# Optimization experiments

Hardware: AMD Instinct MI355X
Metric: run time of the kernel (lower is better)

Reference implementation:

```python
import jax, jax.numpy as jnp
import numpy as np
from jax import lax

T = 8  # primary_vec_length


def setup_inputs() -> dict:
    key = jax.random.key(0)
    k1, k2, k3 = jax.random.split(key, 3)
    x = jax.random.normal(k1, (32, 256, 64, 64), dtype=jnp.float32)
    # Conv2d weight [out_ch, in_ch, kH, kW], kaiming-ish scale
    W = jax.random.normal(k2, (32, 256, 9, 9), dtype=jnp.float32) * 0.01
    b = jax.random.normal(k3, (32,), dtype=jnp.float32) * 0.01
    return {"x": x, "W": W, "b": b}


def reference(x, W, b):
    B = x.shape[0]
    # Conv2d(kernel=9, stride=2, valid). The original applies this conv T times
    # to identical stacked copies of x; compute it once and broadcast (same math).
    conv = lax.conv_general_dilated(
        x, W, window_strides=(2, 2), padding="VALID",
        dimension_numbers=("NCHW", "OIHW", "NCHW"))
    conv = conv + b[None, :, None, None]            # [B, C, H', W']
    s = jnp.broadcast_to(conv[:, None], (B, T) + conv.shape[1:])  # [B, T, C, H', W']
    # squash along dim=1 (the capsule-vector / time dim)
    sq = jnp.sum(s * s, axis=1, keepdims=True)      # [B, 1, C, H', W']
    scale = sq / (1.0 + sq) / jnp.sqrt(sq + 1e-8)
    squ = s * scale                                  # [B, T, C, H', W']
    squ = squ.reshape(B, T, -1)                      # [B, T, C*H'*W']
    squ = jnp.transpose(squ, (0, 2, 1))[..., None]   # [B, N, T, 1]
    return squ
```

## Files before the change

### kernel.cpp

```cpp
#include <hip/hip_runtime.h>
#include <hip/hip_bf16.h>
#include <stdint.h>

typedef _Float16 f16;
typedef _Float16 f16x8 __attribute__((ext_vector_type(8)));
typedef float f32x16 __attribute__((ext_vector_type(16)));
typedef float f32x4 __attribute__((ext_vector_type(4)));
typedef uint32_t u32x4 __attribute__((ext_vector_type(4)));
typedef uint32_t u32x2 __attribute__((ext_vector_type(2)));

#define MFMA(A, B, C) __builtin_amdgcn_mfma_f32_32x32x16_f16((A), (B), (C), 0, 0, 0)

__global__ __launch_bounds__(256) void nchw_to_nhwc_f16(
    const float* __restrict__ x, f16* __restrict__ xt) {
  __shared__ __align__(16) uint32_t tile[64 * 128];
  const int bh = blockIdx.x;
  const int t = threadIdx.x;
  const float* src = x + (size_t)(bh >> 6) * (256 * 4096) + (bh & 63) * 64;

  const int w4 = t & 15;
  const int cq = t >> 4;
  const int xorv = 4 * (w4 & 7);
#pragma unroll
  for (int it = 0; it < 4; ++it) {
    const int c0 = it * 64 + cq * 4;
    float4 v0 = *(const float4*)(src + (size_t)(c0 + 0) * 4096 + w4 * 4);
    float4 v1 = *(const float4*)(src + (size_t)(c0 + 1) * 4096 + w4 * 4);
    float4 v2 = *(const float4*)(src + (size_t)(c0 + 2) * 4096 + w4 * 4);
    float4 v3 = *(const float4*)(src + (size_t)(c0 + 3) * 4096 + w4 * 4);
    const float* p0 = (const float*)&v0;
    const float* p1 = (const float*)&v1;
    const float* p2 = (const float*)&v2;
    const float* p3 = (const float*)&v3;
    const int u = it * 32 + cq * 2;
#pragma unroll
    for (int jw = 0; jw < 4; ++jw) {
      f16 h0 = (f16)p0[jw], h1 = (f16)p1[jw], h2 = (f16)p2[jw], h3 = (f16)p3[jw];
      uint32_t lo = (uint32_t)__builtin_bit_cast(uint16_t, h0) |
                    ((uint32_t)__builtin_bit_cast(uint16_t, h1) << 16);
      uint32_t hi = (uint32_t)__builtin_bit_cast(uint16_t, h2) |
                    ((uint32_t)__builtin_bit_cast(uint16_t, h3) << 16);
      u32x2 pk = {lo, hi};
      const int w = w4 * 4 + jw;
      *(u32x2*)&tile[w * 128 + (u ^ xorv)] = pk;
    }
  }
  __syncthreads();
  f16* dstb = xt + (size_t)bh * 16384;
#pragma unroll
  for (int it = 0; it < 8; ++it) {
    const int n = it * 256 + t;
    const int w2 = n & 31;
    const int par = (n >> 5) & 1;
    const int g8 = n >> 6;
    const int w = par + 2 * w2;
    const u32x4 v = *(const u32x4*)&tile[w * 128 + ((g8 * 4) ^ (4 * ((w >> 2) & 7)))];
    *(u32x4*)(dstb + n * 8) = v;
  }
}

__global__ __launch_bounds__(256) void pack_w(const float* __restrict__ W,
                                              f16* __restrict__ wt) {
  __shared__ float lds[10368];
  const int t = threadIdx.x;
  const int co = blockIdx.x >> 1;
  const int cih = blockIdx.x & 1;
  const float* src = W + (size_t)(co * 256 + cih * 128) * 81;
  for (int i = t; i < 10368; i += 256) lds[i] = src[i];
  __syncthreads();
  for (int j = t; j < 1296; j += 256) {
    const int kk = j >> 4;
    const int t16 = j & 15;
    const int cicl = t16 >> 2;
    const int sg = t16 & 3;
    const int cin = ((sg >> 1) & 1) * 16 + (sg & 1) * 8;
    f16 tmp[8];
#pragma unroll
    for (int e = 0; e < 8; ++e)
      tmp[e] = (f16)lds[(cicl * 32 + cin + e) * 81 + kk];
    const int cic = cih * 4 + cicl;
    *(f16x8*)&wt[(size_t)(((kk * 8 + cic) * 4 + sg) * 32 + co) * 8] = *(f16x8*)tmp;
  }
}

__global__ __launch_bounds__(256, 2) void conv_direct(
    const f16* __restrict__ xt, const f16* __restrict__ wt,
    float* __restrict__ convp) {
  __shared__ __align__(16) char stg[4 * 18432];
  const int tid = threadIdx.x;
  const int lane = tid & 63;
  const int wave = tid >> 6;
  const int m = lane & 31;
  const int hh = lane >> 5;

  const int blk = blockIdx.x;
  const int xcd = blk & 7;
  const int r = blk >> 3;
  const int i4 = r >> 5;
  const int rr = r & 31;
  const int og = rr >> 3;
  const int cic = rr & 7;
  const int bimg = xcd * 4 + i4;
  const int ohp = og * 4 + wave;
  const bool active = (ohp < 14);

  const char* xb = (const char*)xt;
  const char* wb = (const char*)wt;

  const char* ab = xb + ((size_t)(bimg * 64 + 4 * ohp) * 32768 +
                         cic * 4096 + hh * 1024 + m * 16);
  const size_t cic2048 = (size_t)cic * 2048;
  const int fragoff = hh * 512 + m * 16;

#define GLDS(G, L)                                                            \
  __builtin_amdgcn_global_load_lds(                                           \
      (const __attribute__((address_space(1))) void*)(G),                     \
      (__attribute__((address_space(3))) void*)(L), 16, 0, 0)

#define ALOAD(AB, KW, P) \
  (*(const f16x8*)((AB) + (P) * 2048 + ((KW) & 1) * 512 + ((KW) >> 1) * 16))
#define LDSF(P) (*(const f16x8*)(P))

#define STAGE(JN)                                                             \
  {                                                                           \
    const int kkb = (JN) * 9;                                                 \
    char* db = stg + ((JN) & 3) * 18432;                                      \
    _Pragma("unroll") for (int i = 0; i < 4; ++i) {                           \
      const int u = tid + 256 * i;                                            \
      GLDS(wb + (size_t)(kkb + (u >> 7)) * 16384 + cic2048 + (u & 127) * 16,  \
           db + u * 16);                                                      \
    }                                                                         \
    if (tid < 128) {                                                          \
      GLDS(wb + (size_t)(kkb + 8) * 16384 + cic2048 + tid * 16,               \
           db + 16384 + tid * 16);                                            \
    }                                                                         \
  }

  f32x16 acc0, acc1;
#pragma unroll
  for (int i = 0; i < 16; ++i) { acc0[i] = 0.f; acc1[i] = 0.f; }

  STAGE(0)

  for (int j = 0; j < 11; ++j) {
    __syncthreads();
    if (j < 8) STAGE(j + 1)
    if (active) {
      const char* s0 = stg + (j & 3) * 18432 + fragoff;
      const char* s1 = stg + ((j + 2) & 3) * 18432 + fragoff;
      if (j >= 2 && j <= 8) {
#pragma unroll
        for (int kw = 0; kw < 9; ++kw) {
          const f16x8 a0 = ALOAD(ab, kw, 0), a1 = ALOAD(ab, kw, 1);
          acc0 = MFMA(a0, LDSF(s0 + kw * 2048), acc0);
          acc0 = MFMA(a1, LDSF(s0 + kw * 2048 + 1024), acc0);
          acc1 = MFMA(a0, LDSF(s1 + kw * 2048), acc1);
          acc1 = MFMA(a1, LDSF(s1 + kw * 2048 + 1024), acc1);
        }
      } else if (j < 2) {
#pragma unroll
        for (int kw = 0; kw < 9; ++kw) {
          const f16x8 a0 = ALOAD(ab, kw, 0), a1 = ALOAD(ab, kw, 1);
          acc0 = MFMA(a0, LDSF(s0 + kw * 2048), acc0);
          acc0 = MFMA(a1, LDSF(s0 + kw * 2048 + 1024), acc0);
        }
      } else {
#pragma unroll
        for (int kw = 0; kw < 9; ++kw) {
          const f16x8 a0 = ALOAD(ab, kw, 0), a1 = ALOAD(ab, kw, 1);
          acc1 = MFMA(a0, LDSF(s1 + kw * 2048), acc1);
          acc1 = MFMA(a1, LDSF(s1 + kw * 2048 + 1024), acc1);
        }
      }
    }
    ab += 32768;
  }
#undef STAGE
#undef ALOAD
#undef LDSF
#undef GLDS

  if (active) {
#pragma unroll
    for (int tile = 0; tile < 2; ++tile) {
      const int oh = 2 * ohp + tile;
      float* cp = convp + (size_t)cic * 802816 +
                  ((size_t)bimg * 784 + oh * 28) * 32 + m;
      const f32x16& a = tile ? acc1 : acc0;
#pragma unroll
      for (int rI = 0; rI < 16; ++rI) {
        const int ow = (rI & 3) + 8 * (rI >> 2) + 4 * hh;
        if (ow < 28) cp[ow * 32] = a[rI];
      }
    }
  }
}

__global__ __launch_bounds__(256) void epilogue(const float* __restrict__ convp,
                                                const float* __restrict__ bias,
                                                float* __restrict__ out) {
  const int gi = blockIdx.x * 256 + threadIdx.x;
  const int base = gi * 8;
  const int p = gi >> 2;
  const int co0 = (gi & 3) * 8;
  const int bi = p / 784;
  const int pix = p - bi * 784;
  f32x4 v0 = {0.f, 0.f, 0.f, 0.f}, v1 = {0.f, 0.f, 0.f, 0.f};
#pragma unroll
  for (int qq = 0; qq < 8; ++qq) {
    v0 += *(const f32x4*)&convp[(size_t)qq * 802816 + base];
    v1 += *(const f32x4*)&convp[(size_t)qq * 802816 + base + 4];
  }
  float vb[8];
#pragma unroll
  for (int jj = 0; jj < 4; ++jj) {
    vb[jj] = v0[jj] + bias[co0 + jj];
    vb[4 + jj] = v1[jj] + bias[co0 + 4 + jj];
  }
  float* ob = out + (size_t)bi * 200704 + pix * 8;
#pragma unroll
  for (int jj = 0; jj < 8; ++jj) {
    const float vv = vb[jj];
    const float sq = 8.f * vv * vv;
    const float scale = sq / ((1.f + sq) * sqrtf(sq + 1e-8f));
    const float y = vv * scale;
    const f32x4 qv = {y, y, y, y};
    float* o = ob + (size_t)(co0 + jj) * 6272;
    *(f32x4*)o = qv;
    *(f32x4*)(o + 4) = qv;
  }
}

extern "C" void kernel_launch(void* const* d_in, const int* in_sizes, int n_in,
                              void* d_out, int out_size, void* d_ws,
                              size_t ws_size, hipStream_t stream) {
  const float* x = (const float*)d_in[0];
  const float* W = (const float*)d_in[1];
  const float* bias = (const float*)d_in[2];
  float* out = (float*)d_out;

  char* ws = (char*)d_ws;
  f16* xt = (f16*)ws;
  f16* wt = (f16*)(ws + 67108864);
  float* convp = (float*)(ws + 67108864 + 1327104);

  nchw_to_nhwc_f16<<<dim3(2048), dim3(256), 0, stream>>>(x, xt);
  pack_w<<<dim3(64), dim3(256), 0, stream>>>(W, wt);
  conv_direct<<<dim3(1024), dim3(256), 0, stream>>>(xt, wt, convp);
  epilogue<<<dim3(392), dim3(256), 0, stream>>>(convp, bias, out);
}
```

Measured before the change: 285.5 us.

## Restructure conv blocks to cover all output rows and reuse weight fragments in registers

Each conv block now handles all 14 output-row pairs of one image/channel-chunk in two phases, with each wave computing two row pairs. Weight fragments are loaded once from LDS into a 3-deep register ring and reused across both row pairs and both output rows, so weights are staged from global memory far fewer times. The LDS staging shrinks to double buffering, the grid goes from 1024 to 256 blocks, and occupancy drops to one block per CU. The cost is much higher register pressure (large bs array plus four accumulators) and fewer blocks in flight to hide latency.

```diff
diff --git a/kernel.cpp b/kernel.cpp
--- a/kernel.cpp
+++ b/kernel.cpp
@@ -83,10 +83,10 @@
   }
 }
 
-__global__ __launch_bounds__(256, 2) void conv_direct(
+__global__ __launch_bounds__(256, 1) void conv_direct(
     const f16* __restrict__ xt, const f16* __restrict__ wt,
     float* __restrict__ convp) {
-  __shared__ __align__(16) char stg[4 * 18432];
+  __shared__ __align__(16) char stg[2 * 18432];
   const int tid = threadIdx.x;
   const int lane = tid & 63;
   const int wave = tid >> 6;
@@ -95,20 +95,12 @@
 
   const int blk = blockIdx.x;
   const int xcd = blk & 7;
-  const int r = blk >> 3;
-  const int i4 = r >> 5;
-  const int rr = r & 31;
-  const int og = rr >> 3;
-  const int cic = rr & 7;
+  const int i4 = (blk >> 3) & 3;
+  const int cic = blk >> 5;
   const int bimg = xcd * 4 + i4;
-  const int ohp = og * 4 + wave;
-  const bool active = (ohp < 14);
 
   const char* xb = (const char*)xt;
   const char* wb = (const char*)wt;
-
-  const char* ab = xb + ((size_t)(bimg * 64 + 4 * ohp) * 32768 +
-                         cic * 4096 + hh * 1024 + m * 16);
   const size_t cic2048 = (size_t)cic * 2048;
   const int fragoff = hh * 512 + m * 16;
 
@@ -119,12 +111,11 @@
 
 #define ALOAD(AB, KW, P) \
   (*(const f16x8*)((AB) + (P) * 2048 + ((KW) & 1) * 512 + ((KW) >> 1) * 16))
-#define LDSF(P) (*(const f16x8*)(P))
 
 #define STAGE(JN)                                                             \
   {                                                                           \
     const int kkb = (JN) * 9;                                                 \
-    char* db = stg + ((JN) & 3) * 18432;                                      \
+    char* db = stg + ((JN) & 1) * 18432;                                      \
     _Pragma("unroll") for (int i = 0; i < 4; ++i) {                           \
       const int u = tid + 256 * i;                                            \
       GLDS(wb + (size_t)(kkb + (u >> 7)) * 16384 + cic2048 + (u & 127) * 16,  \
@@ -136,64 +127,80 @@
     }                                                                         \
   }
 
-  f32x16 acc0, acc1;
-#pragma unroll
-  for (int i = 0; i < 16; ++i) { acc0[i] = 0.f; acc1[i] = 0.f; }
-
-  STAGE(0)
-
-  for (int j = 0; j < 11; ++j) {
-    __syncthreads();
-    if (j < 8) STAGE(j + 1)
-    if (active) {
-      const char* s0 = stg + (j & 3) * 18432 + fragoff;
-      const char* s1 = stg + ((j + 2) & 3) * 18432 + fragoff;
-      if (j >= 2 && j <= 8) {
+  for (int phase = 0; phase < 2; ++phase) {
+    const int pp0 = phase * 8 + wave;
+    const int pp1 = pp0 + 4;
+    const bool act0 = pp0 < 14;
+    const bool act1 = pp1 < 14;
+    const int pp1c = act1 ? pp1 : pp0;
+    const char* ab0 = xb + ((size_t)(bimg * 64 + 4 * pp0) * 32768 +
+                            cic * 4096 + hh * 1024 + m * 16);
+    const char* ab1 = xb + ((size_t)(bimg * 64 + 4 * pp1c) * 32768 +
+                            cic * 4096 + hh * 1024 + m * 16);
+
+    f32x16 acc00, acc01, acc10, acc11;
+#pragma unroll
+    for (int i = 0; i < 16; ++i) {
+      acc00[i] = 0.f; acc01[i] = 0.f; acc10[i] = 0.f; acc11[i] = 0.f;
+    }
+
+    f16x8 bs[3][18];
+
+    STAGE(0)
+
+#pragma unroll
+    for (int j = 0; j < 11; ++j) {
+      __syncthreads();
+      if (j < 8) STAGE(j + 1)
+      if (j <= 8) {
+        const char* sb = stg + (j & 1) * 18432 + fragoff;
 #pragma unroll
         for (int kw = 0; kw < 9; ++kw) {
-          const f16x8 a0 = ALOAD(ab, kw, 0), a1 = ALOAD(ab, kw, 1);
-          acc0 = MFMA(a0, LDSF(s0 + kw * 2048), acc0);
-          acc0 = MFMA(a1, LDSF(s0 + kw * 2048 + 1024), acc0);
-          acc1 = MFMA(a0, LDSF(s1 + kw * 2048), acc1);
-          acc1 = MFMA(a1, LDSF(s1 + kw * 2048 + 1024), acc1);
-        }
-      } else if (j < 2) {
-#pragma unroll
-        for (int kw = 0; kw < 9; ++kw) {
-          const f16x8 a0 = ALOAD(ab, kw, 0), a1 = ALOAD(ab, kw, 1);
-          acc0 = MFMA(a0, LDSF(s0 + kw * 2048), acc0);
-          acc0 = MFMA(a1, LDSF(s0 + kw * 2048 + 1024), acc0);
-        }
-      } else {
-#pragma unroll
-        for (int kw = 0; kw < 9; ++kw) {
-          const f16x8 a0 = ALOAD(ab, kw, 0), a1 = ALOAD(ab, kw, 1);
-          acc1 = MFMA(a0, LDSF(s1 + kw * 2048), acc1);
-          acc1 = MFMA(a1, LDSF(s1 + kw * 2048 + 1024), acc1);
+          bs[j % 3][2 * kw] = *(const f16x8*)(sb + kw * 2048);
+          bs[j % 3][2 * kw + 1] = *(const f16x8*)(sb + kw * 2048 + 1024);
         }
       }
-    }
-    ab += 32768;
+      const char* aj0 = ab0 + (size_t)j * 32768;
+      const char* aj1 = ab1 + (size_t)j * 32768;
+#pragma unroll
+      for (int kw = 0; kw < 9; ++kw) {
+        const f16x8 a00 = ALOAD(aj0, kw, 0), a01 = ALOAD(aj0, kw, 1);
+        const f16x8 a10 = ALOAD(aj1, kw, 0), a11 = ALOAD(aj1, kw, 1);
+        if (j <= 8) {
+          acc00 = MFMA(a00, bs[j % 3][2 * kw], acc00);
+          acc00 = MFMA(a01, bs[j % 3][2 * kw + 1], acc00);
+          acc10 = MFMA(a10, bs[j % 3][2 * kw], acc10);
+          acc10 = MFMA(a11, bs[j % 3][2 * kw + 1], acc10);
+        }
+        if (j >= 2) {
+          acc01 = MFMA(a00, bs[(j + 1) % 3][2 * kw], acc01);
+          acc01 = MFMA(a01, bs[(j + 1) % 3][2 * kw + 1], acc01);
+          acc11 = MFMA(a10, bs[(j + 1) % 3][2 * kw], acc11);
+          acc11 = MFMA(a11, bs[(j + 1) % 3][2 * kw + 1], acc11);
+        }
+      }
+    }
+
+#define STORE_PAIR(PP, ACT, A0, A1)                                           \
+    if (ACT) {                                                                \
+      _Pragma("unroll") for (int tile = 0; tile < 2; ++tile) {                \
+        const int oh = 2 * (PP) + tile;                                       \
+        float* cp = convp + (size_t)cic * 802816 +                            \
+                    ((size_t)bimg * 784 + oh * 28) * 32 + m;                  \
+        const f32x16& a = tile ? (A1) : (A0);                                 \
+        _Pragma("unroll") for (int rI = 0; rI < 16; ++rI) {                   \
+          const int ow = (rI & 3) + 8 * (rI >> 2) + 4 * hh;                   \
+          if (ow < 28) cp[ow * 32] = a[rI];                                   \
+        }                                                                     \
+      }                                                                       \
+    }
+    STORE_PAIR(pp0, act0, acc00, acc01)
+    STORE_PAIR(pp1, act1, acc10, acc11)
+#undef STORE_PAIR
   }
 #undef STAGE
 #undef ALOAD
-#undef LDSF
 #undef GLDS
-
-  if (active) {
-#pragma unroll
-    for (int tile = 0; tile < 2; ++tile) {
-      const int oh = 2 * ohp + tile;
-      float* cp = convp + (size_t)cic * 802816 +
-                  ((size_t)bimg * 784 + oh * 28) * 32 + m;
-      const f32x16& a = tile ? acc1 : acc0;
-#pragma unroll
-      for (int rI = 0; rI < 16; ++rI) {
-        const int ow = (rI & 3) + 8 * (rI >> 2) + 4 * hh;
-        if (ow < 28) cp[ow * 32] = a[rI];
-      }
-    }
-  }
 }
 
 __global__ __launch_bounds__(256) void epilogue(const float* __restrict__ convp,
@@ -246,6 +253,6 @@
 
   nchw_to_nhwc_f16<<<dim3(2048), dim3(256), 0, stream>>>(x, xt);
   pack_w<<<dim3(64), dim3(256), 0, stream>>>(W, wt);
-  conv_direct<<<dim3(1024), dim3(256), 0, stream>>>(xt, wt, convp);
+  conv_direct<<<dim3(256), dim3(256), 0, stream>>>(xt, wt, convp);
   epilogue<<<dim3(392), dim3(256), 0, stream>>>(convp, bias, out);
 }
```

Result: no change. 289.5 us (+1.4%).

## Compute two output-row pairs per wave to reuse staged weights

Applied to the files above, without the earlier changes.

Each wave now computes two output row-pairs (A and B) instead of one, which halves the conv grid from 1024 to 512 blocks. Every weight fragment loaded from LDS now feeds twice as many MFMAs, so the redundant weight staging across blocks is cut. It also software-pipelines the global A-operand loads one kw step ahead. In exchange it doubles the accumulator registers and lowers block count. The B pair is clamped to A when out of range, which wastes compute for some waves.

```diff
diff --git a/kernel.cpp b/kernel.cpp
--- a/kernel.cpp
+++ b/kernel.cpp
@@ -96,19 +96,24 @@
   const int blk = blockIdx.x;
   const int xcd = blk & 7;
   const int r = blk >> 3;
-  const int i4 = r >> 5;
-  const int rr = r & 31;
+  const int i4 = r >> 4;
+  const int rr = r & 15;
   const int og = rr >> 3;
   const int cic = rr & 7;
   const int bimg = xcd * 4 + i4;
-  const int ohp = og * 4 + wave;
-  const bool active = (ohp < 14);
+
+  const int ohpA = og * 8 + wave;
+  const int ohpB = ohpA + 4;
+  const bool actB = (ohpB < 14);
+  const int ohpBc = actB ? ohpB : ohpA;
 
   const char* xb = (const char*)xt;
   const char* wb = (const char*)wt;
 
-  const char* ab = xb + ((size_t)(bimg * 64 + 4 * ohp) * 32768 +
-                         cic * 4096 + hh * 1024 + m * 16);
+  const char* ab0 = xb + ((size_t)(bimg * 64 + 4 * ohpA) * 32768 +
+                          cic * 4096 + hh * 1024 + m * 16);
+  const char* ab1 = xb + ((size_t)(bimg * 64 + 4 * ohpBc) * 32768 +
+                          cic * 4096 + hh * 1024 + m * 16);
   const size_t cic2048 = (size_t)cic * 2048;
   const int fragoff = hh * 512 + m * 16;
 
@@ -136,64 +141,92 @@
     }                                                                         \
   }
 
-  f32x16 acc0, acc1;
-#pragma unroll
-  for (int i = 0; i < 16; ++i) { acc0[i] = 0.f; acc1[i] = 0.f; }
+  f32x16 accA0, accA1, accB0, accB1;
+#pragma unroll
+  for (int i = 0; i < 16; ++i) {
+    accA0[i] = 0.f; accA1[i] = 0.f; accB0[i] = 0.f; accB1[i] = 0.f;
+  }
 
   STAGE(0)
 
   for (int j = 0; j < 11; ++j) {
     __syncthreads();
     if (j < 8) STAGE(j + 1)
-    if (active) {
-      const char* s0 = stg + (j & 3) * 18432 + fragoff;
-      const char* s1 = stg + ((j + 2) & 3) * 18432 + fragoff;
-      if (j >= 2 && j <= 8) {
-#pragma unroll
-        for (int kw = 0; kw < 9; ++kw) {
-          const f16x8 a0 = ALOAD(ab, kw, 0), a1 = ALOAD(ab, kw, 1);
-          acc0 = MFMA(a0, LDSF(s0 + kw * 2048), acc0);
-          acc0 = MFMA(a1, LDSF(s0 + kw * 2048 + 1024), acc0);
-          acc1 = MFMA(a0, LDSF(s1 + kw * 2048), acc1);
-          acc1 = MFMA(a1, LDSF(s1 + kw * 2048 + 1024), acc1);
+    const char* s0 = stg + (j & 3) * 18432 + fragoff;
+    const char* s1 = stg + ((j + 2) & 3) * 18432 + fragoff;
+    f16x8 a00 = ALOAD(ab0, 0, 0), a01 = ALOAD(ab0, 0, 1);
+    f16x8 a10 = ALOAD(ab1, 0, 0), a11 = ALOAD(ab1, 0, 1);
+    if (j >= 2 && j <= 8) {
+#pragma unroll
+      for (int kw = 0; kw < 9; ++kw) {
+        f16x8 n00, n01, n10, n11;
+        if (kw < 8) {
+          n00 = ALOAD(ab0, kw + 1, 0); n01 = ALOAD(ab0, kw + 1, 1);
+          n10 = ALOAD(ab1, kw + 1, 0); n11 = ALOAD(ab1, kw + 1, 1);
         }
-      } else if (j < 2) {
-#pragma unroll
-        for (int kw = 0; kw < 9; ++kw) {
-          const f16x8 a0 = ALOAD(ab, kw, 0), a1 = ALOAD(ab, kw, 1);
-          acc0 = MFMA(a0, LDSF(s0 + kw * 2048), acc0);
-          acc0 = MFMA(a1, LDSF(s0 + kw * 2048 + 1024), acc0);
+        const f16x8 b00 = LDSF(s0 + kw * 2048);
+        const f16x8 b01 = LDSF(s0 + kw * 2048 + 1024);
+        const f16x8 b10 = LDSF(s1 + kw * 2048);
+        const f16x8 b11 = LDSF(s1 + kw * 2048 + 1024);
+        accA0 = MFMA(a00, b00, accA0); accA0 = MFMA(a01, b01, accA0);
+        accB0 = MFMA(a10, b00, accB0); accB0 = MFMA(a11, b01, accB0);
+        accA1 = MFMA(a00, b10, accA1); accA1 = MFMA(a01, b11, accA1);
+        accB1 = MFMA(a10, b10, accB1); accB1 = MFMA(a11, b11, accB1);
+        a00 = n00; a01 = n01; a10 = n10; a11 = n11;
+      }
+    } else if (j < 2) {
+#pragma unroll
+      for (int kw = 0; kw < 9; ++kw) {
+        f16x8 n00, n01, n10, n11;
+        if (kw < 8) {
+          n00 = ALOAD(ab0, kw + 1, 0); n01 = ALOAD(ab0, kw + 1, 1);
+          n10 = ALOAD(ab1, kw + 1, 0); n11 = ALOAD(ab1, kw + 1, 1);
         }
-      } else {
-#pragma unroll
-        for (int kw = 0; kw < 9; ++kw) {
-          const f16x8 a0 = ALOAD(ab, kw, 0), a1 = ALOAD(ab, kw, 1);
-          acc1 = MFMA(a0, LDSF(s1 + kw * 2048), acc1);
-          acc1 = MFMA(a1, LDSF(s1 + kw * 2048 + 1024), acc1);
+        const f16x8 b00 = LDSF(s0 + kw * 2048);
+        const f16x8 b01 = LDSF(s0 + kw * 2048 + 1024);
+        accA0 = MFMA(a00, b00, accA0); accA0 = MFMA(a01, b01, accA0);
+        accB0 = MFMA(a10, b00, accB0); accB0 = MFMA(a11, b01, accB0);
+        a00 = n00; a01 = n01; a10 = n10; a11 = n11;
+      }
+    } else {
+#pragma unroll
+      for (int kw = 0; kw < 9; ++kw) {
+        f16x8 n00, n01, n10, n11;
+        if (kw < 8) {
+          n00 = ALOAD(ab0, kw + 1, 0); n01 = ALOAD(ab0, kw + 1, 1);
+          n10 = ALOAD(ab1, kw + 1, 0); n11 = ALOAD(ab1, kw + 1, 1);
         }
+        const f16x8 b10 = LDSF(s1 + kw * 2048);
+        const f16x8 b11 = LDSF(s1 + kw * 2048 + 1024);
+        accA1 = MFMA(a00, b10, accA1); accA1 = MFMA(a01, b11, accA1);
+        accB1 = MFMA(a10, b10, accB1); accB1 = MFMA(a11, b11, accB1);
+        a00 = n00; a01 = n01; a10 = n10; a11 = n11;
       }
     }
-    ab += 32768;
+    ab0 += 32768;
+    ab1 += 32768;
   }
 #undef STAGE
 #undef ALOAD
 #undef LDSF
 #undef GLDS
 
-  if (active) {
-#pragma unroll
-    for (int tile = 0; tile < 2; ++tile) {
-      const int oh = 2 * ohp + tile;
-      float* cp = convp + (size_t)cic * 802816 +
-                  ((size_t)bimg * 784 + oh * 28) * 32 + m;
-      const f32x16& a = tile ? acc1 : acc0;
-#pragma unroll
-      for (int rI = 0; rI < 16; ++rI) {
-        const int ow = (rI & 3) + 8 * (rI >> 2) + 4 * hh;
-        if (ow < 28) cp[ow * 32] = a[rI];
-      }
-    }
-  }
+#define STORE_PAIR(PP, ACT, A0, A1)                                           \
+  if (ACT) {                                                                  \
+    _Pragma("unroll") for (int tile = 0; tile < 2; ++tile) {                  \
+      const int oh = 2 * (PP) + tile;                                         \
+      float* cp = convp + (size_t)cic * 802816 +                              \
+                  ((size_t)bimg * 784 + oh * 28) * 32 + m;                    \
+      const f32x16& a = tile ? (A1) : (A0);                                   \
+      _Pragma("unroll") for (int rI = 0; rI < 16; ++rI) {                     \
+        const int ow = (rI & 3) + 8 * (rI >> 2) + 4 * hh;                     \
+        if (ow < 28) cp[ow * 32] = a[rI];                                     \
+      }                                                                       \
+    }                                                                         \
+  }
+  STORE_PAIR(ohpA, true, accA0, accA1)
+  STORE_PAIR(ohpB, actB, accB0, accB1)
+#undef STORE_PAIR
 }
 
 __global__ __launch_bounds__(256) void epilogue(const float* __restrict__ convp,
@@ -246,6 +279,6 @@
 
   nchw_to_nhwc_f16<<<dim3(2048), dim3(256), 0, stream>>>(x, xt);
   pack_w<<<dim3(64), dim3(256), 0, stream>>>(W, wt);
-  conv_direct<<<dim3(1024), dim3(256), 0, stream>>>(xt, wt, convp);
+  conv_direct<<<dim3(512), dim3(256), 0, stream>>>(xt, wt, convp);
   epilogue<<<dim3(392), dim3(256), 0, stream>>>(convp, bias, out);
 }
```

New measurement: 282.5 us. No clear change (-1.1%).
